# Kernel optimization log

Hardware: AMD Instinct MI355X
Metric: run time of the kernel (lower is better)

Reference implementation:

```python
import jax, jax.numpy as jnp
import numpy as np

DT = 0.01
NLAG = 50           # int(maxlag / dt), maxlag = 0.5 s
NMA = 20
NC = 8192
NT = 4096


def _xcorr(data1, data2):
    # torch F.conv1d(data1.view(1, nc, nt), data2.view(nc, 1, nt),
    #                padding=NLAG+1, groups=nc)
    # == per-channel sliding cross-correlation.
    lhs = data1[None]            # (1, NC, NT)
    rhs = data2[:, None, :]      # (NC, 1, NT) -- one tiny filter per group
    out = jax.lax.conv_general_dilated(
        lhs, rhs,
        window_strides=(1,),
        padding=[(NLAG + 1, NLAG + 1)],
        dimension_numbers=("NCH", "OIH", "NCH"),
        feature_group_count=NC,
    )
    return out                   # (1, NC, L), L = 2*NLAG + 3 when nt1 == nt2


def _moving_average(x, nma=NMA):
    # Faithful to CCModel.moving_average: AvgPool1d(nma, stride=1, pad=nma//2)
    # applied after permute(0,2,1), i.e. the pooling runs over the CHANNEL
    # axis, with zero padding included in the mean (count_include_pad=True),
    # then sliced back to nc channels.
    nb, nc, L = x.shape
    pad = nma // 2
    xp = jnp.pad(x, ((0, 0), (pad, pad), (0, 0)))
    cs = jnp.concatenate(
        [jnp.zeros((nb, 1, L), x.dtype), jnp.cumsum(xp, axis=1)], axis=1)
    win = (cs[:, nma:, :] - cs[:, :-nma, :]) / nma   # sliding sum / nma
    return win[:, :nc, :]


def _pick_maxabs(R, dt):
    # pick_Rkt_maxabs: per-channel max-|cc| pick.
    L = R.shape[-1]
    nlag_c = (L - 1) // 2        # zero-lag index
    imax = jnp.argmax(jnp.abs(R), axis=-1)                              # (nb, nc)
    vmain = jnp.take_along_axis(R, imax[..., None], axis=-1)[..., 0]    # signed peak
    vpos = jnp.max(R, axis=-1)
    vneg = jnp.min(R, axis=-1)
    vside = jnp.where(vmain >= 0, vneg, vpos)        # opposite-sign extremum
    tmax = (imax - nlag_c).astype(R.dtype) * dt
    return vmain, vside, tmax


def setup_inputs() -> dict:
    key = jax.random.key(0)
    k1, k2, k3, k4 = jax.random.split(key, 4)
    data1 = jax.random.normal(k1, (NC, NT), dtype=jnp.float32)
    data2 = jax.random.normal(k2, (NC, NT), dtype=jnp.float32)
    event1 = jax.random.randint(k3, (1,), 0, 1000, dtype=jnp.int32)
    event2 = jax.random.randint(k4, (1,), 0, 1000, dtype=jnp.int32)
    return {"data1": data1, "data2": data2, "event1": event1, "event2": event2}


def reference(data1, data2, event1, event2):
    xcor = _xcorr(data1, data2)              # (1, NC, 2*NLAG+3)
    xcor = _moving_average(xcor, NMA)        # in-place overwrite in torch
    vmax, vmin, tmax = _pick_maxabs(xcor, DT)
    return xcor, vmax, vmin, tmax
```

## Files before the change

kernel.cpp:

```cpp
#include <hip/hip_runtime.h>

#define NC 8192
#define NT 4096
#define NLAGS 103
#define WS_STRIDE 104
#define XBASE (NC*NLAGS)

__device__ __forceinline__ int Pg(int q) {
    return (q & ~127) | ((q & 7) << 4) | ((q >> 3) & 15);
}
__device__ __forceinline__ int Pinv(int p) {
    return (p & ~127) | ((p & 15) << 3) | ((p >> 4) & 7);
}

#define D1GR 1152
#define D2GR 1024
#define SMEMDW ((D1GR + D2GR)*4)
#define REDS 29

__global__ __launch_bounds__(256, 4)
void xcorr_kernel(const float* __restrict__ g1, const float* __restrict__ g2,
                  float* __restrict__ ws) {
    __shared__ __align__(128) float smem[SMEMDW];
    char* d1b = (char*)smem;
    char* d2b = (char*)smem + D1GR*16;
    const int tid  = threadIdx.x;
    const int wv   = tid >> 6;
    const int lane = tid & 63;
    const int c    = blockIdx.x;
    const float* g1c = g1 + (size_t)c * NT;
    const float* g2c = g2 + (size_t)c * NT;

    #pragma unroll
    for (int t = 0; t < 4; ++t) {
        const int j = 4*wv + t;
        const int q = Pinv(64*j + lane);
        __builtin_amdgcn_global_load_lds(
            (const float*)((const char*)g2c + 16*q),
            (float*)(d2b + 1024*j),
            16, 0, 0);
    }

    #pragma unroll
    for (int t = 0; t < 5; ++t) {
        const int p = tid + 256*t;
        if (p < D1GR) {
            const int q = Pinv(p);
            float4 v = make_float4(0.f, 0.f, 0.f, 0.f);
            if (q >= 13 && q < 1037)
                v = *(const float4*)((const char*)g1c + 16*q - 208);
            *(float4*)(d1b + 16*p) = v;
        }
    }
    __syncthreads();

    float acc[28];
    #pragma unroll
    for (int l = 0; l < 28; ++l) acc[l] = 0.f;

    #pragma unroll 1
    for (int it = 0; it < 2; ++it) {
        const int qb = 512*it + 8*lane;
        const int qa = qb + 7*wv;
        #pragma unroll
        for (int h = 0; h < 2; ++h) {
            float b[16];
            #pragma unroll
            for (int t = 0; t < 4; ++t) {
                float4 v = *(const float4*)(d2b + 16*Pg(qb + 4*h + t));
                b[4*t]=v.x; b[4*t+1]=v.y; b[4*t+2]=v.z; b[4*t+3]=v.w;
            }
            float w[44];
            #pragma unroll
            for (int t = 0; t < 11; ++t) {
                float4 v = *(const float4*)(d1b + 16*Pg(qa + 4*h + t));
                w[4*t]=v.x; w[4*t+1]=v.y; w[4*t+2]=v.z; w[4*t+3]=v.w;
            }
            #pragma unroll
            for (int j = 0; j < 16; ++j)
                #pragma unroll
                for (int l = 0; l < 28; ++l)
                    acc[l] = fmaf(w[l+j], b[j], acc[l]);
            __builtin_amdgcn_sched_barrier(0);
        }
    }

    __syncthreads();
    #pragma unroll
    for (int l = 0; l < 28; ++l) acc[l] += __shfl_down(acc[l], 32);
    float* red = (float*)d2b + wv * (32*REDS);
    if (lane < 32) {
        #pragma unroll
        for (int l = 0; l < 28; ++l) red[lane*REDS + l] = acc[l];
    }
    if (lane < 28) {
        float s = 0.f;
        #pragma unroll
        for (int r = 0; r < 32; ++r) s += red[r*REDS + lane];
        const int L = 28*wv + lane - 1;
        if (L >= 0 && L < NLAGS) ws[(size_t)c * WS_STRIDE + L] = s;
    }
}

#define TS 112
__global__ __launch_bounds__(256, 4)
void ma_pick_kernel(const float* __restrict__ ws, float* __restrict__ out) {
    __shared__ float tile[52*TS];
    __shared__ float matile[32*TS];
    const int tid = threadIdx.x;
    const int c0  = blockIdx.x * 32;

    for (int i = tid; i < 52*TS; i += 256) {
        int r   = i / TS;
        int col = i - r*TS;
        int g   = c0 - 10 + r;
        float v = 0.f;
        if (g >= 0 && g < NC && col < NLAGS) v = ws[(size_t)g*WS_STRIDE + col];
        tile[i] = v;
    }
    __syncthreads();

    {
        const int l = tid & 127;
        const int h = tid >> 7;
        if (l < NLAGS) {
            const int cc0 = h * 16;
            float s = 0.f;
            #pragma unroll
            for (int r = 0; r < 20; ++r) s += tile[(cc0 + r)*TS + l];
            #pragma unroll 1
            for (int cc = cc0; cc < cc0 + 16; ++cc) {
                float ma = s / 20.0f;
                matile[cc*TS + l] = ma;
                out[(size_t)(c0 + cc)*NLAGS + l] = ma;
                s += tile[(cc + 20)*TS + l] - tile[cc*TS + l];
            }
        }
    }
    __syncthreads();

    const int wv = tid >> 6, lane = tid & 63;
    #pragma unroll 1
    for (int s8 = 0; s8 < 8; ++s8) {
        const int cc = wv*8 + s8;
        float v1 = matile[cc*TS + lane];
        float a1 = fabsf(v1);
        int   i1 = lane;
        float vmx = v1, vmn = v1;
        if (lane < NLAGS - 64) {
            float v2 = matile[cc*TS + 64 + lane];
            float a2 = fabsf(v2);
            vmx = fmaxf(vmx, v2); vmn = fminf(vmn, v2);
            if (a2 > a1) { a1 = a2; i1 = 64 + lane; v1 = v2; }
        }
        #pragma unroll
        for (int d = 32; d >= 1; d >>= 1) {
            float oa  = __shfl_xor(a1, d);
            int   oi  = __shfl_xor(i1, d);
            float ov  = __shfl_xor(v1, d);
            float omx = __shfl_xor(vmx, d);
            float omn = __shfl_xor(vmn, d);
            vmx = fmaxf(vmx, omx);
            vmn = fminf(vmn, omn);
            if (oa > a1 || (oa == a1 && oi < i1)) { a1 = oa; i1 = oi; v1 = ov; }
        }
        if (lane == 0) {
            const int ch = c0 + cc;
            out[XBASE + ch]        = v1;
            out[XBASE + NC + ch]   = (v1 >= 0.f) ? vmn : vmx;
            out[XBASE + 2*NC + ch] = (float)(i1 - 51) * 0.01f;
        }
    }
}

extern "C" void kernel_launch(void* const* d_in, const int* in_sizes, int n_in,
                              void* d_out, int out_size, void* d_ws, size_t ws_size,
                              hipStream_t stream) {
    const float* g1 = (const float*)d_in[0];
    const float* g2 = (const float*)d_in[1];
    float* out = (float*)d_out;
    float* ws  = (float*)d_ws;

    hipLaunchKernelGGL(xcorr_kernel, dim3(NC), dim3(256), 0, stream, g1, g2, ws);
    hipLaunchKernelGGL(ma_pick_kernel, dim3(NC/32), dim3(256), 0, stream, ws, out);
}
```

Before: 316.5 us.

## Stream data2 from global into registers and widen per-wave lag tile

The kernel no longer stages data2 in LDS through global_load_lds. Each lane now loads its 32-float slice of data2 straight into registers, double-buffered so the next chunk's load overlaps the current phase's FMAs. The LDS layout for data1 becomes a simpler 8-way strided permutation, and each wave now covers 32 lags instead of 28 with a fully unrolled 4-phase schedule. This roughly halves the LDS footprint and drops the data2 LDS reads. In exchange, global loads are strided across lanes, more registers are live, and extra lags are computed and then discarded.

```diff
diff --git a/kernel.cpp b/kernel.cpp
--- a/kernel.cpp
+++ b/kernel.cpp
@@ -6,46 +6,57 @@
 #define WS_STRIDE 104
 #define XBASE (NC*NLAGS)
 
-__device__ __forceinline__ int Pg(int q) {
-    return (q & ~127) | ((q & 7) << 4) | ((q >> 3) & 15);
-}
-__device__ __forceinline__ int Pinv(int p) {
-    return (p & ~127) | ((p & 15) << 3) | ((p >> 4) & 7);
-}
+#define D1GR 1152
+#define SMEMDW (D1GR*4)
+#define REDS 33
 
-#define D1GR 1152
-#define D2GR 1024
-#define SMEMDW ((D1GR + D2GR)*4)
-#define REDS 29
+#define OFFG(t) (2304*((t)&7) + 16*((t)>>3))
+
+#define LOADB(OFF, B0,B1,B2,B3) do { \
+    B0 = *(const float4*)(b0p + (OFF));      B1 = *(const float4*)(b0p + (OFF) + 4); \
+    B2 = *(const float4*)(b0p + (OFF) + 8);  B3 = *(const float4*)(b0p + (OFF) + 12); \
+} while(0)
+
+#define PHASE(VB, H, C0,C1,C2,C3) do { \
+    float w[48]; \
+    _Pragma("unroll") \
+    for (int t = 0; t < 12; ++t) { \
+        float4 v = *(const float4*)((VB) + OFFG(4*(H) + t)); \
+        w[4*t+0]=v.x; w[4*t+1]=v.y; w[4*t+2]=v.z; w[4*t+3]=v.w; \
+    } \
+    float b[16]; \
+    b[0]=C0.x; b[1]=C0.y; b[2]=C0.z; b[3]=C0.w; \
+    b[4]=C1.x; b[5]=C1.y; b[6]=C1.z; b[7]=C1.w; \
+    b[8]=C2.x; b[9]=C2.y; b[10]=C2.z; b[11]=C2.w; \
+    b[12]=C3.x; b[13]=C3.y; b[14]=C3.z; b[15]=C3.w; \
+    _Pragma("unroll") \
+    for (int j = 0; j < 16; ++j) \
+        _Pragma("unroll") \
+        for (int l = 0; l < 32; ++l) \
+            acc[l] = fmaf(w[l+j], b[j], acc[l]); \
+} while(0)
 
 __global__ __launch_bounds__(256, 4)
 void xcorr_kernel(const float* __restrict__ g1, const float* __restrict__ g2,
                   float* __restrict__ ws) {
-    __shared__ __align__(128) float smem[SMEMDW];
+    __shared__ __align__(16) float smem[SMEMDW];
     char* d1b = (char*)smem;
-    char* d2b = (char*)smem + D1GR*16;
     const int tid  = threadIdx.x;
     const int wv   = tid >> 6;
     const int lane = tid & 63;
     const int c    = blockIdx.x;
     const float* g1c = g1 + (size_t)c * NT;
     const float* g2c = g2 + (size_t)c * NT;
+    const float* b0p = g2c + 32*lane;
+
+    float4 Ba0,Ba1,Ba2,Ba3, Bb0,Bb1,Bb2,Bb3;
+    LOADB(0, Ba0,Ba1,Ba2,Ba3);
 
     #pragma unroll
-    for (int t = 0; t < 4; ++t) {
-        const int j = 4*wv + t;
-        const int q = Pinv(64*j + lane);
-        __builtin_amdgcn_global_load_lds(
-            (const float*)((const char*)g2c + 16*q),
-            (float*)(d2b + 1024*j),
-            16, 0, 0);
-    }
-
-    #pragma unroll
-    for (int t = 0; t < 5; ++t) {
-        const int p = tid + 256*t;
+    for (int s = 0; s < 5; ++s) {
+        const int p = tid + 256*s;
         if (p < D1GR) {
-            const int q = Pinv(p);
+            const int q = 8*(p % 144) + (p / 144);
             float4 v = make_float4(0.f, 0.f, 0.f, 0.f);
             if (q >= 13 && q < 1037)
                 v = *(const float4*)((const char*)g1c + 16*q - 208);
@@ -54,50 +65,32 @@
     }
     __syncthreads();
 
-    float acc[28];
+    float acc[32];
     #pragma unroll
-    for (int l = 0; l < 28; ++l) acc[l] = 0.f;
+    for (int l = 0; l < 32; ++l) acc[l] = 0.f;
 
-    #pragma unroll 1
-    for (int it = 0; it < 2; ++it) {
-        const int qb = 512*it + 8*lane;
-        const int qa = qb + 7*wv;
-        #pragma unroll
-        for (int h = 0; h < 2; ++h) {
-            float b[16];
-            #pragma unroll
-            for (int t = 0; t < 4; ++t) {
-                float4 v = *(const float4*)(d2b + 16*Pg(qb + 4*h + t));
-                b[4*t]=v.x; b[4*t+1]=v.y; b[4*t+2]=v.z; b[4*t+3]=v.w;
-            }
-            float w[44];
-            #pragma unroll
-            for (int t = 0; t < 11; ++t) {
-                float4 v = *(const float4*)(d1b + 16*Pg(qa + 4*h + t));
-                w[4*t]=v.x; w[4*t+1]=v.y; w[4*t+2]=v.z; w[4*t+3]=v.w;
-            }
-            #pragma unroll
-            for (int j = 0; j < 16; ++j)
-                #pragma unroll
-                for (int l = 0; l < 28; ++l)
-                    acc[l] = fmaf(w[l+j], b[j], acc[l]);
-            __builtin_amdgcn_sched_barrier(0);
-        }
-    }
+    const char* vb0 = d1b + 16*(lane + wv);
+    const char* vb1 = vb0 + 1024;
+
+    LOADB(16,   Bb0,Bb1,Bb2,Bb3);
+    PHASE(vb0, 0, Ba0,Ba1,Ba2,Ba3);
+    LOADB(2048, Ba0,Ba1,Ba2,Ba3);
+    PHASE(vb0, 1, Bb0,Bb1,Bb2,Bb3);
+    LOADB(2064, Bb0,Bb1,Bb2,Bb3);
+    PHASE(vb1, 0, Ba0,Ba1,Ba2,Ba3);
+    PHASE(vb1, 1, Bb0,Bb1,Bb2,Bb3);
 
     __syncthreads();
     #pragma unroll
-    for (int l = 0; l < 28; ++l) acc[l] += __shfl_down(acc[l], 32);
-    float* red = (float*)d2b + wv * (32*REDS);
+    for (int l = 0; l < 32; ++l) acc[l] += __shfl_down(acc[l], 32);
+    float* red = smem + wv * (32*REDS);
     if (lane < 32) {
         #pragma unroll
-        for (int l = 0; l < 28; ++l) red[lane*REDS + l] = acc[l];
-    }
-    if (lane < 28) {
+        for (int l = 0; l < 32; ++l) red[lane*REDS + l] = acc[l];
         float s = 0.f;
         #pragma unroll
         for (int r = 0; r < 32; ++r) s += red[r*REDS + lane];
-        const int L = 28*wv + lane - 1;
+        const int L = 32*wv + lane - 1;
         if (L >= 0 && L < NLAGS) ws[(size_t)c * WS_STRIDE + L] = s;
     }
 }
```

Measured after the change: 342.7 us. 1.08x slower.
